# Optimization experiments

Hardware: AMD Instinct MI355X
Metric: run time of the kernel (lower is better)

Reference implementation:

```python
import jax, jax.numpy as jnp
import numpy as np

WS = 4          # window_size
NH = 4          # num_heads
HID = 192       # hidden_dim
IN_DIM = 64     # input_dim
GROUPS = 8      # min(8, hidden_dim)
EPS = 1e-5


def layer_norm(x, g, b):
    mu = jnp.mean(x, axis=-1, keepdims=True)
    var = jnp.var(x, axis=-1, keepdims=True)
    return (x - mu) * jax.lax.rsqrt(var + EPS) * g + b


def group_norm(x, g, b):
    # x: [B, C, H, W], groups over channels
    B, C, H, W = x.shape
    xg = x.reshape(B, GROUPS, C // GROUPS, H, W)
    mu = jnp.mean(xg, axis=(2, 3, 4), keepdims=True)
    var = jnp.var(xg, axis=(2, 3, 4), keepdims=True)
    xn = ((xg - mu) * jax.lax.rsqrt(var + EPS)).reshape(B, C, H, W)
    return xn * g[None, :, None, None] + b[None, :, None, None]


def setup_inputs() -> dict:
    key = jax.random.key(0)
    ks = jax.random.split(key, 16)
    B, H, W = 8, 128, 128
    s = lambda *shape: 0.02
    inp = {
        "x": jax.random.normal(ks[0], (B, IN_DIM, H, W), jnp.float32),
        "h": jax.random.normal(ks[1], (B, HID, H, W), jnp.float32),
        "c": jax.random.normal(ks[2], (B, HID, H, W), jnp.float32),
        # in_proj: Conv2d(input_dim+hidden_dim -> hidden_dim, 1x1)
        "w_in": jax.random.normal(ks[3], (HID, IN_DIM + HID), jnp.float32) * 0.02,
        "b_in": jnp.zeros((HID,), jnp.float32),
        # LocalWindowAttention params
        "ln_g": jnp.ones((HID,), jnp.float32),
        "ln_b": jnp.zeros((HID,), jnp.float32),
        "w_qkv": jax.random.normal(ks[4], (3 * HID, HID), jnp.float32) * 0.02,
        "b_qkv": jnp.zeros((3 * HID,), jnp.float32),
        "w_proj": jax.random.normal(ks[5], (HID, HID), jnp.float32) * 0.02,
        "b_proj": jnp.zeros((HID,), jnp.float32),
        # GroupNorm (shared: applied to attn_map and hnext)
        "gn_g": jnp.ones((HID,), jnp.float32),
        "gn_b": jnp.zeros((HID,), jnp.float32),
        # gates_conv: Conv2d(hidden_dim -> 4*hidden_dim, 1x1)
        "w_gates": jax.random.normal(ks[6], (4 * HID, HID), jnp.float32) * 0.02,
        "b_gates": jnp.zeros((4 * HID,), jnp.float32),
    }
    return inp


def reference(x, h, c, w_in, b_in, ln_g, ln_b, w_qkv, b_qkv,
              w_proj, b_proj, gn_g, gn_b, w_gates, b_gates):
    B, _, H, W = x.shape
    C = HID
    hd = C // NH
    scale = hd ** -0.5

    # in_proj (1x1 conv == channel GEMM)
    comb = jnp.concatenate([x, h], axis=1)
    proj = jnp.einsum('oc,bchw->bohw', w_in, comb) + b_in[None, :, None, None]

    # H, W are multiples of WS -> no reflect padding (matches torch common path)
    nh, nw = H // WS, W // WS
    # window_partition: [B, C, H, W] -> [B*nh*nw, WS*WS, C]
    xw = proj.reshape(B, C, nh, WS, nw, WS).transpose(0, 2, 4, 3, 5, 1)
    xw = xw.reshape(B * nh * nw, WS * WS, C)

    # LocalWindowAttention
    xn = layer_norm(xw, ln_g, ln_b)
    qkv = xn @ w_qkv.T + b_qkv                       # [Bw, N, 3C]
    Bw, N, _ = qkv.shape
    qkv = qkv.reshape(Bw, N, 3, NH, hd)
    q = qkv[:, :, 0].transpose(0, 2, 1, 3)           # [Bw, NH, N, hd]
    k = qkv[:, :, 1].transpose(0, 2, 1, 3)
    v = qkv[:, :, 2].transpose(0, 2, 1, 3)
    attn = jax.nn.softmax(jnp.einsum('bhnd,bhmd->bhnm', q, k) * scale, axis=-1)
    out = jnp.einsum('bhnm,bhmd->bhnd', attn, v)
    out = out.transpose(0, 2, 1, 3).reshape(Bw, N, C)
    out = out @ w_proj.T + b_proj

    # window_unpartition: [B*nh*nw, WS*WS, C] -> [B, C, H, W]
    amap = out.reshape(B, nh, nw, WS, WS, C).transpose(0, 5, 1, 3, 2, 4)
    amap = amap.reshape(B, C, H, W)

    amap = group_norm(amap, gn_g, gn_b)

    # gates (1x1 conv) + LSTM cell math
    gates = jnp.einsum('oc,bchw->bohw', w_gates, amap) + b_gates[None, :, None, None]
    ci, cf, co, cg = jnp.split(gates, 4, axis=1)
    i = jax.nn.sigmoid(ci)
    f = jax.nn.sigmoid(cf)
    o = jax.nn.sigmoid(co)
    g = jnp.tanh(cg)
    cnext = f * c + i * g
    hnext = o * jnp.tanh(cnext)
    hnext = group_norm(hnext, gn_g, gn_b)
    return (hnext, cnext)
```

## Files before the change

kernel.cpp:

```cpp
#include <hip/hip_runtime.h>

#define HW 16384
#define W_IMG 128
#define CH 192
#define CIN 64
#define P_TOT 131072
#define EPS 1e-5f

__device__ __forceinline__ void blockReduce2(float& a, float& b2, float* lds) {
#pragma unroll
  for (int off = 32; off > 0; off >>= 1) {
    a  += __shfl_down(a,  off, 64);
    b2 += __shfl_down(b2, off, 64);
  }
  int wv = threadIdx.x >> 6, ln = threadIdx.x & 63;
  if (ln == 0) { lds[wv] = a; lds[4 + wv] = b2; }
  __syncthreads();
  if (threadIdx.x == 0) {
    a  = lds[0] + lds[1] + lds[2] + lds[3];
    b2 = lds[4] + lds[5] + lds[6] + lds[7];
  }
}

__global__ __launch_bounds__(256) void k0_prep(
    const float* __restrict__ w_g, float* __restrict__ wT)
{
  int idx = blockIdx.x * 256 + threadIdx.x;
  if (idx < 147456) {
    int row = idx / 192, c = idx - row * 192;
    wT[(size_t)c * 768 + row] = w_g[idx];
  }
}

__global__ __launch_bounds__(256) void k3_fused(
    const float* __restrict__ x,  const float* __restrict__ h,
    const float* __restrict__ w_in, const float* __restrict__ b_in,
    const float* __restrict__ ln_g, const float* __restrict__ ln_b,
    const float* __restrict__ w_qkv, const float* __restrict__ b_qkv,
    const float* __restrict__ w_proj, const float* __restrict__ b_proj,
    float* __restrict__ amap)
{
  __shared__ float qk[6144];
  __shared__ float xnb[3072];
  __shared__ float scr[544];
  const int tid = threadIdx.x;
  const int wid = blockIdx.x;
  const int b  = wid >> 10;
  const int wy = (wid >> 5) & 31;
  const int wx = wid & 31;
  const int pix0 = (wy * 4) * W_IMG + wx * 4;

  for (int idx = tid; idx < 1024; idx += 256) {
    int cch = idx >> 2, ty = idx & 3;
    const float* src = (cch < 64)
        ? x + (size_t)(b * CIN + cch) * HW + pix0 + ty * W_IMG
        : h + (size_t)(b * CH + (cch - 64)) * HW + pix0 + ty * W_IMG;
    const float4 v = *(const float4*)src;
    float* d = &qk[cch * 16 + ty * 4];
    d[0] = v.x; d[1] = v.y; d[2] = v.z; d[3] = v.w;
  }
  __syncthreads();

  if (tid < 192) {
    const int j = tid;
    float acc[16];
    float bj = b_in[j];
#pragma unroll
    for (int t = 0; t < 16; ++t) acc[t] = bj;
    const float* wr = w_in + (size_t)j * 256;
#pragma unroll 4
    for (int c = 0; c < 256; ++c) {
      float wv = wr[c];
      const float* xr = &qk[c * 16];
#pragma unroll
      for (int t = 0; t < 16; ++t) acc[t] = fmaf(wv, xr[t], acc[t]);
    }
    float* o = &xnb[j * 16];
#pragma unroll
    for (int t = 0; t < 16; ++t) o[t] = acc[t];
  }
  __syncthreads();

  {
    int g = tid >> 4, t = tid & 15;
    float s = 0.f, s2 = 0.f;
    const float* p = &xnb[g * 12 * 16 + t];
#pragma unroll
    for (int jj = 0; jj < 12; ++jj) { float v = p[jj * 16]; s += v; s2 = fmaf(v, v, s2); }
    scr[tid] = s; scr[256 + tid] = s2;
  }
  __syncthreads();
  if (tid < 16) {
    float s = 0.f, s2 = 0.f;
#pragma unroll
    for (int g = 0; g < 16; ++g) { s += scr[g * 16 + tid]; s2 += scr[256 + g * 16 + tid]; }
    float mu = s * (1.f / 192.f);
    float var = s2 * (1.f / 192.f) - mu * mu;
    scr[512 + tid] = mu;
    scr[528 + tid] = rsqrtf(fmaxf(var, 0.f) + EPS);
  }
  __syncthreads();

  for (int idx = tid; idx < 3072; idx += 256) {
    int j = idx >> 4, t = idx & 15;
    xnb[idx] = (xnb[idx] - scr[512 + t]) * scr[528 + t] * ln_g[j] + ln_b[j];
  }
  __syncthreads();

  for (int r = 0; r < 3; ++r) {
    int idx = r * 256 + tid;
    int j = idx >> 1, th = idx & 1;
    float bj = b_qkv[j];
    float acc[8];
#pragma unroll
    for (int i = 0; i < 8; ++i) acc[i] = bj;
    const float* wr = w_qkv + (size_t)j * 192;
    const float* xr = &xnb[th * 8];
#pragma unroll 4
    for (int c = 0; c < 192; ++c) {
      float wv = wr[c];
      const float* xc = xr + c * 16;
#pragma unroll
      for (int i = 0; i < 8; ++i) acc[i] = fmaf(wv, xc[i], acc[i]);
    }
    float* o = &qk[j * 16 + th * 8];
#pragma unroll
    for (int i = 0; i < 8; ++i) o[i] = acc[i];
  }
  __syncthreads();

  const float scale = 0.14433756729740643f;
#pragma unroll
  for (int p = 0; p < 2; ++p) {
    for (int r = 0; r < 2; ++r) {
      int idx = r * 256 + tid;
      int hhl = idx >> 8, t1 = (idx >> 4) & 15, t2 = idx & 15;
      int hh = 2 * p + hhl;
      const float* qq = &qk[(hh * 48) * 16 + t1];
      const float* kk = &qk[3072 + (hh * 48) * 16 + t2];
      float sv = 0.f;
#pragma unroll
      for (int d = 0; d < 48; ++d) sv = fmaf(qq[d * 16], kk[d * 16], sv);
      scr[(hhl * 16 + t1) * 17 + t2] = sv * scale;
    }
    __syncthreads();
    if (tid < 128) {
      int rrow = tid >> 2, i = tid & 3;
      const float* row = &scr[rrow * 17 + i * 4];
      float v0 = row[0], v1 = row[1], v2 = row[2], v3 = row[3];
      float m = fmaxf(fmaxf(v0, v1), fmaxf(v2, v3));
      m = fmaxf(m, __shfl_xor(m, 1));
      m = fmaxf(m, __shfl_xor(m, 2));
      float e0 = __expf(v0 - m), e1 = __expf(v1 - m);
      float e2 = __expf(v2 - m), e3 = __expf(v3 - m);
      float s = e0 + e1 + e2 + e3;
      s += __shfl_xor(s, 1);
      s += __shfl_xor(s, 2);
      float inv = 1.f / s;
      float* pd = &qk[(p * 32 + rrow) * 17 + i * 4];
      pd[0] = e0 * inv; pd[1] = e1 * inv; pd[2] = e2 * inv; pd[3] = e3 * inv;
    }
    __syncthreads();
  }

  if (tid < 192) {
    const int j = tid;
    float acc[16];
    float bj = b_qkv[384 + j];
#pragma unroll
    for (int t = 0; t < 16; ++t) acc[t] = bj;
    const float* wr = w_qkv + (size_t)(384 + j) * 192;
#pragma unroll 4
    for (int c = 0; c < 192; ++c) {
      float wv = wr[c];
      const float* xr = &xnb[c * 16];
#pragma unroll
      for (int t = 0; t < 16; ++t) acc[t] = fmaf(wv, xr[t], acc[t]);
    }
    float* o = &qk[3072 + j * 16];
#pragma unroll
    for (int t = 0; t < 16; ++t) o[t] = acc[t];
  }
  __syncthreads();

  for (int r = 0; r < 12; ++r) {
    int idx = r * 256 + tid;
    int cc = idx >> 4, t = idx & 15;
    const float* pr = &qk[((cc / 48) * 16 + t) * 17];
    const float* vr = &qk[3072 + cc * 16];
    float sv = 0.f;
#pragma unroll
    for (int t2 = 0; t2 < 16; ++t2) sv = fmaf(pr[t2], vr[t2], sv);
    xnb[cc * 16 + t] = sv;
  }
  __syncthreads();

  if (tid < 192) {
    const int o = tid;
    float acc[16];
    float bo = b_proj[o];
#pragma unroll
    for (int t = 0; t < 16; ++t) acc[t] = bo;
    const float* wr = w_proj + (size_t)o * 192;
#pragma unroll 4
    for (int c = 0; c < 192; ++c) {
      float wv = wr[c];
      const float* xr = &xnb[c * 16];
#pragma unroll
      for (int t = 0; t < 16; ++t) acc[t] = fmaf(wv, xr[t], acc[t]);
    }
    float* op = amap + (size_t)(b * CH + o) * HW + pix0;
#pragma unroll
    for (int ty = 0; ty < 4; ++ty) {
      *(float4*)(op + ty * W_IMG) =
          make_float4(acc[ty * 4], acc[ty * 4 + 1], acc[ty * 4 + 2], acc[ty * 4 + 3]);
    }
  }
}

__global__ __launch_bounds__(256) void k4_stats(
    const float* __restrict__ src, float* __restrict__ stats)
{
  __shared__ float lds[8];
  int blk = blockIdx.x;
  int chunk = blk & 15, bc = blk >> 4;
  int b = bc / 192, cch = bc % 192;
  const float4 v = *(const float4*)(src + (size_t)bc * HW + chunk * 1024 + threadIdx.x * 4);
  float s  = v.x + v.y + v.z + v.w;
  float s2 = v.x * v.x + v.y * v.y + v.z * v.z + v.w * v.w;
  blockReduce2(s, s2, lds);
  if (threadIdx.x == 0) {
    atomicAdd(&stats[(b * 8 + cch / 24) * 2],     s);
    atomicAdd(&stats[(b * 8 + cch / 24) * 2 + 1], s2);
  }
}

__global__ __launch_bounds__(256) void k4b_scale(
    const float* __restrict__ stats, const float* __restrict__ gn_g,
    const float* __restrict__ gn_b, float* __restrict__ scaleS, float* __restrict__ shiftS)
{
  int idx = blockIdx.x * 256 + threadIdx.x;
  if (idx >= 1536) return;
  int b = idx / 192, cch = idx % 192, g = cch / 24;
  float n = 24.f * HW;
  float mu  = stats[(b * 8 + g) * 2] / n;
  float var = stats[(b * 8 + g) * 2 + 1] / n - mu * mu;
  float rs = rsqrtf(fmaxf(var, 0.f) + EPS);
  float scl = rs * gn_g[cch];
  scaleS[idx] = scl;
  shiftS[idx] = gn_b[cch] - mu * scl;
}

__global__ __launch_bounds__(256) void k6_gates(
    float* __restrict__ outp,
    const float* __restrict__ wT,
    const float* __restrict__ b_g, const float* __restrict__ cin,
    const float* __restrict__ scaleS, const float* __restrict__ shiftS)
{
  __shared__ float tile[192 * 64];
  const int tid = threadIdx.x;
  const int b  = blockIdx.x >> 8;
  const int s0 = (blockIdx.x & 255) * 64;
  float* cout = outp + (size_t)P_TOT * CH;

  for (int idx = tid; idx < 12288; idx += 256) {
    int c = idx >> 6, p = idx & 63;
    float raw = outp[(size_t)(b * CH + c) * HW + s0 + p];
    tile[idx] = fmaf(raw, scaleS[b * CH + c], shiftS[b * CH + c]);
  }
  __syncthreads();

  const int lane = tid & 63;
  const int wv = __builtin_amdgcn_readfirstlane(tid >> 6);

  for (int jg = wv * 6; jg < wv * 6 + 6; ++jg) {
    const int j0 = jg * 8;
    float acc[32];
#pragma unroll
    for (int k = 0; k < 4; ++k)
#pragma unroll
      for (int r = 0; r < 8; ++r) acc[k * 8 + r] = b_g[k * 192 + j0 + r];
#pragma unroll 2
    for (int c = 0; c < 192; ++c) {
      float a = tile[c * 64 + lane];
      const float* wc = wT + (size_t)c * 768 + j0;
#pragma unroll
      for (int k = 0; k < 4; ++k)
#pragma unroll
        for (int r = 0; r < 8; ++r)
          acc[k * 8 + r] = fmaf(a, wc[k * 192 + r], acc[k * 8 + r]);
    }
#pragma unroll
    for (int r = 0; r < 8; ++r) {
      size_t base = (size_t)(b * CH + j0 + r) * HW + s0 + lane;
      float ci = acc[r], cf = acc[8 + r], co = acc[16 + r], cg = acc[24 + r];
      float iv = 1.f / (1.f + __expf(-ci));
      float fv = 1.f / (1.f + __expf(-cf));
      float ov = 1.f / (1.f + __expf(-co));
      float gv = 1.f - 2.f / (__expf(2.f * cg) + 1.f);
      float cn = fmaf(fv, cin[base], iv * gv);
      cout[base] = cn;
      float th = 1.f - 2.f / (__expf(2.f * cn) + 1.f);
      outp[base] = ov * th;
    }
  }
}

__global__ __launch_bounds__(256) void k7_hnext(
    const float* __restrict__ stats2,
    const float* __restrict__ gn_g, const float* __restrict__ gn_b,
    float* __restrict__ outp)
{
  int blk = blockIdx.x;
  int chunk = blk & 15, bc = blk >> 4;
  int b = bc / 192, cch = bc % 192, g = cch / 24;
  float n = 24.f * HW;
  float mu  = stats2[(b * 8 + g) * 2] / n;
  float var = stats2[(b * 8 + g) * 2 + 1] / n - mu * mu;
  float rs = rsqrtf(fmaxf(var, 0.f) + EPS);
  float scl = rs * gn_g[cch];
  float shf = gn_b[cch] - mu * scl;
  float* p = outp + (size_t)bc * HW + chunk * 1024 + threadIdx.x * 4;
  float4 v = *(float4*)p;
  v.x = fmaf(v.x, scl, shf); v.y = fmaf(v.y, scl, shf);
  v.z = fmaf(v.z, scl, shf); v.w = fmaf(v.w, scl, shf);
  *(float4*)p = v;
}

extern "C" void kernel_launch(void* const* d_in, const int* in_sizes, int n_in,
                              void* d_out, int out_size, void* d_ws, size_t ws_size,
                              hipStream_t stream) {
  (void)in_sizes; (void)n_in; (void)out_size; (void)ws_size;
  const float* x      = (const float*)d_in[0];
  const float* h      = (const float*)d_in[1];
  const float* c      = (const float*)d_in[2];
  const float* w_in   = (const float*)d_in[3];
  const float* b_in   = (const float*)d_in[4];
  const float* ln_g   = (const float*)d_in[5];
  const float* ln_b   = (const float*)d_in[6];
  const float* w_qkv  = (const float*)d_in[7];
  const float* b_qkv  = (const float*)d_in[8];
  const float* w_proj = (const float*)d_in[9];
  const float* b_proj = (const float*)d_in[10];
  const float* gn_g   = (const float*)d_in[11];
  const float* gn_b   = (const float*)d_in[12];
  const float* w_g    = (const float*)d_in[13];
  const float* b_g    = (const float*)d_in[14];
  float* outp = (float*)d_out;
  char* ws = (char*)d_ws;
  float* wT     = (float*)ws;
  float* statsA = (float*)(ws + 589824);
  float* stats2 = (float*)(ws + 590336);
  float* scaleS = (float*)(ws + 590848);
  float* shiftS = (float*)(ws + 596992);

  hipMemsetAsync(statsA, 0, 1024, stream);

  k0_prep  <<<576, 256, 0, stream>>>(w_g, wT);
  k3_fused <<<8192, 256, 0, stream>>>(x, h, w_in, b_in, ln_g, ln_b,
                                      w_qkv, b_qkv, w_proj, b_proj, outp);
  k4_stats <<<24576, 256, 0, stream>>>(outp, statsA);
  k4b_scale<<<6, 256, 0, stream>>>(statsA, gn_g, gn_b, scaleS, shiftS);
  k6_gates <<<2048, 256, 0, stream>>>(outp, wT, b_g, c, scaleS, shiftS);
  k4_stats <<<24576, 256, 0, stream>>>(outp, stats2);
  k7_hnext <<<24576, 256, 0, stream>>>(stats2, gn_g, gn_b, outp);
}
```

Before: 3.205 ms.

## Split-K register-tiled GEMMs with 3 output rows per thread in fused window-attention kernel

Replaces the per-thread single-row GEMMs in the fused attention kernel with a shared helper. Each group of 4 threads splits the K dimension, each thread computes 3 output rows by 16 pixels, and partial sums are combined with lane shuffles. This uses all 256 threads instead of 192, reuses each LDS activation load across three weight rows, and reads float4 from LDS. Launch bounds now request 4 blocks per CU. The cost is 48 accumulators per thread and extra shuffle reductions, which raises register pressure under the tighter occupancy bound.

```diff
diff --git a/kernel.cpp b/kernel.cpp
--- a/kernel.cpp
+++ b/kernel.cpp
@@ -32,7 +32,64 @@
   }
 }
 
-__global__ __launch_bounds__(256) void k3_fused(
+__device__ __forceinline__ float4 pick4(const float s[16], int kp, float bj) {
+  if (kp == 0) return make_float4(s[0] + bj, s[1] + bj, s[2] + bj, s[3] + bj);
+  if (kp == 1) return make_float4(s[4] + bj, s[5] + bj, s[6] + bj, s[7] + bj);
+  if (kp == 2) return make_float4(s[8] + bj, s[9] + bj, s[10] + bj, s[11] + bj);
+  return make_float4(s[12] + bj, s[13] + bj, s[14] + bj, s[15] + bj);
+}
+
+template<int KCC>
+__device__ __forceinline__ void gemm3(
+    const float* __restrict__ w0, int wld,
+    const float* __restrict__ bias,
+    const float* __restrict__ xin,
+    float* __restrict__ outBase,
+    int rs, int ks,
+    int kp)
+{
+  float acc[3][16];
+#pragma unroll
+  for (int r = 0; r < 3; ++r)
+#pragma unroll
+    for (int t = 0; t < 16; ++t) acc[r][t] = 0.f;
+
+  const float* wp0 = w0 + kp;
+  const float* wp1 = w0 + wld + kp;
+  const float* wp2 = w0 + 2 * wld + kp;
+
+#pragma unroll 2
+  for (int cc = 0; cc < KCC; ++cc) {
+    float wa = wp0[cc * 4];
+    float wb = wp1[cc * 4];
+    float wc = wp2[cc * 4];
+    const float4* xc = (const float4*)&xin[(cc * 4 + kp) << 4];
+    float4 x0 = xc[0], x1 = xc[1], x2 = xc[2], x3 = xc[3];
+    float xv[16] = {x0.x, x0.y, x0.z, x0.w, x1.x, x1.y, x1.z, x1.w,
+                    x2.x, x2.y, x2.z, x2.w, x3.x, x3.y, x3.z, x3.w};
+#pragma unroll
+    for (int t = 0; t < 16; ++t) {
+      acc[0][t] = fmaf(wa, xv[t], acc[0][t]);
+      acc[1][t] = fmaf(wb, xv[t], acc[1][t]);
+      acc[2][t] = fmaf(wc, xv[t], acc[2][t]);
+    }
+  }
+
+#pragma unroll
+  for (int r = 0; r < 3; ++r) {
+#pragma unroll
+    for (int t = 0; t < 16; ++t) {
+      float v = acc[r][t];
+      v += __shfl_xor(v, 1);
+      v += __shfl_xor(v, 2);
+      acc[r][t] = v;
+    }
+    float4 o = pick4(acc[r], kp, bias[r]);
+    *(float4*)&outBase[r * rs + kp * ks] = o;
+  }
+}
+
+__global__ __launch_bounds__(256, 4) void k3_fused(
     const float* __restrict__ x,  const float* __restrict__ h,
     const float* __restrict__ w_in, const float* __restrict__ b_in,
     const float* __restrict__ ln_g, const float* __restrict__ ln_b,
@@ -44,6 +101,8 @@
   __shared__ float xnb[3072];
   __shared__ float scr[544];
   const int tid = threadIdx.x;
+  const int ju  = tid >> 2;
+  const int kp  = tid & 3;
   const int wid = blockIdx.x;
   const int b  = wid >> 10;
   const int wy = (wid >> 5) & 31;
@@ -61,24 +120,8 @@
   }
   __syncthreads();
 
-  if (tid < 192) {
-    const int j = tid;
-    float acc[16];
-    float bj = b_in[j];
-#pragma unroll
-    for (int t = 0; t < 16; ++t) acc[t] = bj;
-    const float* wr = w_in + (size_t)j * 256;
-#pragma unroll 4
-    for (int c = 0; c < 256; ++c) {
-      float wv = wr[c];
-      const float* xr = &qk[c * 16];
-#pragma unroll
-      for (int t = 0; t < 16; ++t) acc[t] = fmaf(wv, xr[t], acc[t]);
-    }
-    float* o = &xnb[j * 16];
-#pragma unroll
-    for (int t = 0; t < 16; ++t) o[t] = acc[t];
-  }
+  gemm3<64>(w_in + (size_t)(3 * ju) * 256, 256, b_in + 3 * ju,
+            qk, &xnb[(3 * ju) * 16], 16, 4, kp);
   __syncthreads();
 
   {
@@ -107,25 +150,11 @@
   }
   __syncthreads();
 
-  for (int r = 0; r < 3; ++r) {
-    int idx = r * 256 + tid;
-    int j = idx >> 1, th = idx & 1;
-    float bj = b_qkv[j];
-    float acc[8];
-#pragma unroll
-    for (int i = 0; i < 8; ++i) acc[i] = bj;
-    const float* wr = w_qkv + (size_t)j * 192;
-    const float* xr = &xnb[th * 8];
-#pragma unroll 4
-    for (int c = 0; c < 192; ++c) {
-      float wv = wr[c];
-      const float* xc = xr + c * 16;
-#pragma unroll
-      for (int i = 0; i < 8; ++i) acc[i] = fmaf(wv, xc[i], acc[i]);
-    }
-    float* o = &qk[j * 16 + th * 8];
-#pragma unroll
-    for (int i = 0; i < 8; ++i) o[i] = acc[i];
+#pragma unroll
+  for (int jp = 0; jp < 2; ++jp) {
+    int j0 = jp * 192 + 3 * ju;
+    gemm3<48>(w_qkv + (size_t)j0 * 192, 192, b_qkv + j0,
+              xnb, &qk[j0 * 16], 16, 4, kp);
   }
   __syncthreads();
 
@@ -163,23 +192,10 @@
     __syncthreads();
   }
 
-  if (tid < 192) {
-    const int j = tid;
-    float acc[16];
-    float bj = b_qkv[384 + j];
-#pragma unroll
-    for (int t = 0; t < 16; ++t) acc[t] = bj;
-    const float* wr = w_qkv + (size_t)(384 + j) * 192;
-#pragma unroll 4
-    for (int c = 0; c < 192; ++c) {
-      float wv = wr[c];
-      const float* xr = &xnb[c * 16];
-#pragma unroll
-      for (int t = 0; t < 16; ++t) acc[t] = fmaf(wv, xr[t], acc[t]);
-    }
-    float* o = &qk[3072 + j * 16];
-#pragma unroll
-    for (int t = 0; t < 16; ++t) o[t] = acc[t];
+  {
+    int j0 = 384 + 3 * ju;
+    gemm3<48>(w_qkv + (size_t)j0 * 192, 192, b_qkv + j0,
+              xnb, &qk[3072 + (3 * ju) * 16], 16, 4, kp);
   }
   __syncthreads();
 
@@ -195,27 +211,8 @@
   }
   __syncthreads();
 
-  if (tid < 192) {
-    const int o = tid;
-    float acc[16];
-    float bo = b_proj[o];
-#pragma unroll
-    for (int t = 0; t < 16; ++t) acc[t] = bo;
-    const float* wr = w_proj + (size_t)o * 192;
-#pragma unroll 4
-    for (int c = 0; c < 192; ++c) {
-      float wv = wr[c];
-      const float* xr = &xnb[c * 16];
-#pragma unroll
-      for (int t = 0; t < 16; ++t) acc[t] = fmaf(wv, xr[t], acc[t]);
-    }
-    float* op = amap + (size_t)(b * CH + o) * HW + pix0;
-#pragma unroll
-    for (int ty = 0; ty < 4; ++ty) {
-      *(float4*)(op + ty * W_IMG) =
-          make_float4(acc[ty * 4], acc[ty * 4 + 1], acc[ty * 4 + 2], acc[ty * 4 + 3]);
-    }
-  }
+  gemm3<48>(w_proj + (size_t)(3 * ju) * 192, 192, b_proj + 3 * ju,
+            xnb, amap + (size_t)(b * CH + 3 * ju) * HW + pix0, HW, W_IMG, kp);
 }
 
 __global__ __launch_bounds__(256) void k4_stats(
```

New measurement: 2.998 ms. -6.4%, faster.
